# Performance work log

Hardware: AMD Instinct MI355X
Metric: run time of the kernel (lower is better)

The kernel has to match this reference:

```python
import jax, jax.numpy as jnp
import numpy as np

B, L, H = 64, 512, 512          # batch, max_len, hidden_size (code requires H == L)
ITEM = 50001                    # item_num + 1
TEMP = 0.2                      # gumbel-sigmoid temperature
EPS = 1e-20


def setup_inputs() -> dict:
    key = jax.random.key(0)
    ks = jax.random.split(key, 16)
    lin = lambda k: jax.random.normal(k, (L, L), jnp.float32) * (1.0 / np.sqrt(L))
    U = jax.random.uniform(ks[13], (L, H), jnp.float32)
    gumbel = -jnp.log(-jnp.log(U + EPS) + EPS)
    return {
        "positives": jax.random.randint(ks[0], (B, L), 0, ITEM),
        "mask": jax.random.randint(ks[1], (B, L), 0, 2).astype(jnp.int32),
        "item_emb": jax.random.normal(ks[2], (ITEM, H), jnp.float32) * 0.02,
        "pos_emb": jax.random.normal(ks[3], (L, H), jnp.float32) * 0.02,
        "Wz": lin(ks[4]),
        "Wv": lin(ks[5]),
        "Wq": lin(ks[6]),
        "Wk": lin(ks[7]),
        "gamma_q": jax.random.normal(ks[8], (L,), jnp.float32) * 0.02,
        "beta_q": jnp.zeros((L,), jnp.float32),
        "gamma_k": jax.random.normal(ks[9], (L,), jnp.float32) * 0.02,
        "beta_k": jnp.zeros((L,), jnp.float32),
        "sparse_w": jax.random.uniform(ks[10], (L, H), jnp.float32, 0.2, 0.8),
        "gumbel": gumbel,
    }


def reference(positives, mask, item_emb, pos_emb, Wz, Wv, Wq, Wk,
              gamma_q, beta_q, gamma_k, beta_k, sparse_w, gumbel):
    # ---- merge_attn_masks: True = masked ----
    pad = ~(mask.astype(bool))[:, None, :]                 # [B,1,L]
    future = jnp.triu(jnp.ones((L, L), bool), k=1)         # strictly upper
    merged = pad | future[None]                            # [B,L,L]
    attn_mask = (~jnp.eye(L, dtype=bool))[None] & merged   # keep diagonal unmasked

    # ---- embeddings ----
    x = item_emb[positives] + pos_emb[None]                # [B,L,H]

    # ---- GAU-style projections (Linear acts on last dim, y = x @ W^T) ----
    z = jax.nn.silu(x @ Wz.T)                              # [B,L,H]
    v = jax.nn.silu(x @ Wv.T)                              # [B,L,H]
    q = (z @ Wq.T) * gamma_q + beta_q                      # OffsetScale head 0
    k = (z @ Wk.T) * gamma_k + beta_k

    # ---- relu^2 attention with bool mask added then zeroed ----
    m = attn_mask.astype(q.dtype)
    a = jnp.einsum('bld,bmd->blm', q, k) + m               # torch adds bool as 0/1
    a = a * (1.0 - m)                                      # a * ~attn_mask

    # ---- gumbel-sigmoid sparse mask (broadcast [L,L] over batch) ----
    smask = jax.nn.sigmoid((jnp.log(sparse_w / (1.0 - sparse_w)) + gumbel) / TEMP)
    a = smask[None] * a

    a = jnp.square(jax.nn.relu(a)) / (L * H)
    return a @ v                                           # [B,L,H]
```

## Files before the change

### kernel.cpp

```cpp
#include <hip/hip_runtime.h>
#include <hip/hip_fp16.h>
#include <math.h>

typedef _Float16 f16;
typedef unsigned int u32;
typedef _Float16 f16x8 __attribute__((ext_vector_type(8)));
typedef _Float16 f16x4 __attribute__((ext_vector_type(4)));
typedef float    f32x4 __attribute__((ext_vector_type(4)));

constexpr int LEN  = 512;
constexpr int HID  = 512;
constexpr int BATCH = 64;

#define BM 128
#define BN 128
#define BK 64

__device__ __forceinline__ void gload16(const f16* g, f16* l) {
    __builtin_amdgcn_global_load_lds((const __attribute__((address_space(1))) u32*)g,
                                     (__attribute__((address_space(3))) u32*)l,
                                     16, 0, 0);
}

__device__ __forceinline__ float silu_f(float v) {
    return v * __builtin_amdgcn_rcpf(1.f + __expf(-v));
}

#define LDSP 272

__device__ __forceinline__ void stage_pass8(const f16* __restrict__ g, f16* l) {
    const int tid = threadIdx.x;
    const int row = tid >> 2;
    const int sc  = (tid & 3) ^ (row & 3);
    gload16(g + (size_t)row * HID + sc * 8, l + (tid >> 6) * 512);
}

__device__ __forceinline__ void stage_tile8(const f16* __restrict__ A,
                                            const f16* __restrict__ B,
                                            int kt, f16* buf) {
    stage_pass8(A + kt * 32,             buf);
    stage_pass8(A + kt * 32 + 128 * HID, buf + 4096);
    stage_pass8(B + kt * 32,             buf + 8192);
    stage_pass8(B + kt * 32 + 128 * HID, buf + 12288);
}

__device__ __forceinline__ void gemm8_core(const f16* __restrict__ A,
                                           const f16* __restrict__ B,
                                           f16* lds, f32x4 acc[8][4])
{
    const int tid  = threadIdx.x;
    const int lane = tid & 63;
    const int wv   = tid >> 6;
    const int wr   = wv >> 2, wc = wv & 3;
    const int mf   = lane & 15;
    const int slot = ((lane >> 4) ^ (mf & 3)) * 8;
    const int aoff = (wr * 128 + mf) * 32 + slot;
    const int boff = (wc * 64  + mf) * 32 + slot + 8192;

    #pragma unroll
    for (int m = 0; m < 8; ++m)
        #pragma unroll
        for (int n = 0; n < 4; ++n)
            acc[m][n] = (f32x4){0.f, 0.f, 0.f, 0.f};

    stage_tile8(A, B, 0, lds);
    stage_tile8(A, B, 1, lds + 16384);
    asm volatile("s_waitcnt vmcnt(4)" ::: "memory");
    __builtin_amdgcn_s_barrier();

    f16x8 af[4], bf[4];
    #pragma unroll
    for (int kt = 0; kt < 16; ++kt) {
        f16* buf  = lds + (kt % 3) * 16384;
        f16* nbuf = lds + ((kt + 2) % 3) * 16384;
        const bool st = (kt < 14);

        #pragma unroll
        for (int m = 0; m < 4; ++m) af[m] = *(const f16x8*)(buf + aoff + m * 512);
        #pragma unroll
        for (int n = 0; n < 4; ++n) bf[n] = *(const f16x8*)(buf + boff + n * 512);
        if (st) {
            stage_pass8(A + (kt + 2) * 32,             nbuf);
            stage_pass8(A + (kt + 2) * 32 + 128 * HID, nbuf + 4096);
        }
        __builtin_amdgcn_s_barrier();
        asm volatile("s_waitcnt lgkmcnt(0)" ::: "memory");
        __builtin_amdgcn_sched_barrier(0);
        __builtin_amdgcn_s_setprio(1);
        #pragma unroll
        for (int m = 0; m < 4; ++m)
            #pragma unroll
            for (int n = 0; n < 4; ++n)
                acc[m][n] = __builtin_amdgcn_mfma_f32_16x16x32_f16(af[m], bf[n], acc[m][n], 0, 0, 0);
        __builtin_amdgcn_s_setprio(0);
        __builtin_amdgcn_s_barrier();

        #pragma unroll
        for (int m = 0; m < 4; ++m) af[m] = *(const f16x8*)(buf + aoff + (m + 4) * 512);
        if (st) {
            stage_pass8(B + (kt + 2) * 32,             nbuf + 8192);
            stage_pass8(B + (kt + 2) * 32 + 128 * HID, nbuf + 12288);
        }
        __builtin_amdgcn_s_barrier();
        asm volatile("s_waitcnt lgkmcnt(0)" ::: "memory");
        __builtin_amdgcn_sched_barrier(0);
        __builtin_amdgcn_s_setprio(1);
        #pragma unroll
        for (int m = 0; m < 4; ++m)
            #pragma unroll
            for (int n = 0; n < 4; ++n)
                acc[m + 4][n] = __builtin_amdgcn_mfma_f32_16x16x32_f16(af[m], bf[n], acc[m + 4][n], 0, 0, 0);
        __builtin_amdgcn_s_setprio(0);
        if (kt < 14)       asm volatile("s_waitcnt vmcnt(4)" ::: "memory");
        else if (kt == 14) asm volatile("s_waitcnt vmcnt(0)" ::: "memory");
        __builtin_amdgcn_s_barrier();
    }
}

__device__ __forceinline__ void store_tile8(const f16* lds, f16* __restrict__ gout, int ldo) {
    const int tid = threadIdx.x;
    #pragma unroll
    for (int ph = 0; ph < 16; ++ph) {
        const int r = ph * 16 + (tid >> 5);
        const int c = (tid & 31) * 8;
        *(f16x8*)(gout + (size_t)r * ldo + c) = *(const f16x8*)(lds + r * LDSP + c);
    }
}

#define EPI8_IDX() \
    const int lane = threadIdx.x & 63, wv_ = threadIdx.x >> 6;  \
    const int wr = wv_ >> 2, wc = wv_ & 3;                      \
    const int c0 = lane & 15, r0 = (lane >> 4) * 4;

__global__ __launch_bounds__(512, 2) void k_zv8(const f16* __restrict__ x,
                                                const f16* __restrict__ Wzh,
                                                const f16* __restrict__ Wvh,
                                                f16* __restrict__ z,
                                                f16* __restrict__ vt)
{
    __shared__ __align__(16) f16 lds[256 * LDSP];
    const int bid = blockIdx.x;
    const int s  = (bid & 7) + 8 * (bid >> 5);
    const int ci = (bid >> 3) & 3;
    const f16* A; const f16* Bm; f16* gout;
    if (ci < 2) {
        A = x + (size_t)s * 256 * HID;
        Bm = Wzh + (size_t)ci * 256 * HID;
        gout = z + (size_t)s * 256 * HID + ci * 256;
    } else {
        const int ht = ci - 2, b = s >> 1, mt = s & 1;
        A = Wvh + (size_t)ht * 256 * HID;
        Bm = x + ((size_t)b * LEN + mt * 256) * HID;
        gout = vt + (size_t)b * HID * LEN + (size_t)ht * 256 * LEN + mt * 256;
    }
    f32x4 acc[8][4];
    gemm8_core(A, Bm, lds, acc);
    __syncthreads();
    {
        EPI8_IDX();
        #pragma unroll
        for (int m = 0; m < 8; ++m)
            #pragma unroll
            for (int n = 0; n < 4; ++n)
                #pragma unroll
                for (int i = 0; i < 4; ++i) {
                    const int row = wr * 128 + m * 16 + r0 + i;
                    const int col = wc * 64 + n * 16 + c0;
                    lds[row * LDSP + col] = (f16)silu_f(acc[m][n][i]);
                }
    }
    __syncthreads();
    store_tile8(lds, gout, 512);
}

__global__ __launch_bounds__(512, 2) void k_qkp8(const f16* __restrict__ z,
                                                 const f16* __restrict__ Wqh,
                                                 const f16* __restrict__ Wkh,
                                                 const float* __restrict__ gq,
                                                 const float* __restrict__ bq,
                                                 const float* __restrict__ gk,
                                                 const float* __restrict__ bk,
                                                 f16* __restrict__ qh,
                                                 f16* __restrict__ kh)
{
    __shared__ __align__(16) f16 lds[256 * LDSP];
    const int bid = blockIdx.x;
    const int s  = (bid & 7) + 8 * (bid >> 5);
    const int ci = (bid >> 3) & 3;
    const bool isq = ci < 2;
    const int nt = isq ? ci : ci - 2;
    const f16* W = isq ? Wqh : Wkh;
    const float* g  = isq ? gq : gk;
    const float* be = isq ? bq : bk;
    f16* outp = isq ? qh : kh;
    f32x4 acc[8][4];
    gemm8_core(z + (size_t)s * 256 * HID, W + (size_t)nt * 256 * HID, lds, acc);
    __syncthreads();
    {
        EPI8_IDX();
        #pragma unroll
        for (int n = 0; n < 4; ++n) {
            const int col = wc * 64 + n * 16 + c0;
            const int jg = nt * 256 + col;
            const float ga = g[jg], ba = be[jg];
            #pragma unroll
            for (int m = 0; m < 8; ++m)
                #pragma unroll
                for (int i = 0; i < 4; ++i) {
                    const int row = wr * 128 + m * 16 + r0 + i;
                    lds[row * LDSP + col] = (f16)((acc[m][n][i] * ga + ba) * 1024.f);
                }
        }
    }
    __syncthreads();
    store_tile8(lds, outp + (size_t)s * 256 * HID + nt * 256, 512);
}

__device__ __forceinline__ void gemm_core(const f16* __restrict__ A, int lda,
                                          const f16* __restrict__ Bm, int ldb,
                                          int ksteps,
                                          f16* ldsA, f16* ldsB,
                                          f32x4 acc[4][4])
{
    const int tid  = threadIdx.x;
    const int lane = tid & 63;
    const int wv   = tid >> 6;
    const int wr   = wv >> 1, wc = wv & 1;
    const int mf   = lane & 15;
    const int kf   = (lane >> 4) * 8;

    for (int r = 0; r < 4; ++r)
        for (int c = 0; c < 4; ++c)
            acc[r][c] = (f32x4){0.f, 0.f, 0.f, 0.f};

    for (int kt = 0; kt < ksteps; ++kt) {
        const int k0 = kt * BK;
        #pragma unroll
        for (int j = 0; j < 4; ++j) {
            const int cb  = j * 256 + wv * 64;
            const int c   = cb + lane;
            const int row = c >> 3;
            const int col = (c & 7) << 3;
            gload16(A  + (size_t)row * lda + (k0 + col), ldsA + cb * 8);
            gload16(Bm + (size_t)row * ldb + (k0 + col), ldsB + cb * 8);
        }
        __syncthreads();
        #pragma unroll
        for (int kk = 0; kk < BK; kk += 32) {
            f16x8 af[4], bf[4];
            #pragma unroll
            for (int r = 0; r < 4; ++r) {
                af[r] = *(const f16x8*)(ldsA + (wr * 64 + r * 16 + mf) * BK + kk + kf);
                bf[r] = *(const f16x8*)(ldsB + (wc * 64 + r * 16 + mf) * BK + kk + kf);
            }
            #pragma unroll
            for (int r = 0; r < 4; ++r)
                #pragma unroll
                for (int c = 0; c < 4; ++c)
                    acc[r][c] = __builtin_amdgcn_mfma_f32_16x16x32_f16(af[r], bf[c], acc[r][c], 0, 0, 0);
        }
        __syncthreads();
    }
}

#define EPILOGUE_IDX() \
    const int lane = threadIdx.x & 63, wv_ = threadIdx.x >> 6;   \
    const int wr = wv_ >> 1, wc = wv_ & 1;                       \
    const int c0 = lane & 15, r0 = (lane >> 4) * 4;

__device__ __forceinline__ void store_tile_f16(f16* lds, const f16 vals[4][4][4],
                                               f16* __restrict__ gout, int ldo)
{
    const int tid = threadIdx.x;
    EPILOGUE_IDX();
    #pragma unroll
    for (int r = 0; r < 4; ++r)
        #pragma unroll
        for (int c = 0; c < 4; ++c)
            #pragma unroll
            for (int i = 0; i < 4; ++i) {
                const int lr = wr * 64 + r * 16 + r0 + i;
                const int lc = wc * 64 + c * 16 + c0;
                lds[lr * 128 + lc] = vals[r][c][i];
            }
    __syncthreads();
    #pragma unroll
    for (int ph = 0; ph < 8; ++ph) {
        const int row = ph * 16 + (tid >> 4);
        const int col = (tid & 15) * 8;
        *(f16x8*)(gout + (size_t)row * ldo + col) = *(const f16x8*)(lds + row * 128 + col);
    }
}

__constant__ int LT_TAB[10] = {0,1,1,2,2,2,3,3,3,3};
__constant__ int MT_TAB[10] = {0,0,1,0,1,2,0,1,2,3};

__global__ __launch_bounds__(256) void k_qk(const f16* __restrict__ q,
                                            const f16* __restrict__ kmat,
                                            const int* __restrict__ mask,
                                            const float* __restrict__ smask,
                                            f16* __restrict__ p)
{
    const int bid = blockIdx.x;
    const int t = (bid >> 3) % 10;
    const int b = (bid & 7) + 8 * (bid / 80);
    const int lt = LT_TAB[t], mt = MT_TAB[t];
    __shared__ f16 lds[(BM + BN) * BK];
    f32x4 acc[4][4];
    const size_t boff = (size_t)b * LEN * HID;
    gemm_core(q + boff + (size_t)lt * BM * HID, HID,
              kmat + boff + (size_t)mt * BN * HID, HID,
              HID / BK, lds, lds + BM * BK, acc);
    f16 vals[4][4][4];
    {
        EPILOGUE_IDX();
        #pragma unroll
        for (int r = 0; r < 4; ++r)
            #pragma unroll
            for (int c = 0; c < 4; ++c) {
                const int m = mt * BN + wc * 64 + c * 16 + c0;
                const int keepcol = mask[b * LEN + m];
                #pragma unroll
                for (int i = 0; i < 4; ++i) {
                    const int l = lt * BM + wr * 64 + r * 16 + r0 + i;
                    const bool keep = (l == m) || ((m <= l) && (keepcol != 0));
                    float v = keep ? acc[r][c][i] * smask[l * LEN + m] : 0.f;
                    v = fmaxf(v, 0.f);
                    vals[r][c][i] = (f16)(v * v);
                }
            }
    }
    store_tile_f16(lds, vals, p + (size_t)b * LEN * LEN + (size_t)lt * BM * LEN + mt * BN, LEN);
}

__global__ __launch_bounds__(256) void k_pv(const f16* __restrict__ p,
                                            const f16* __restrict__ vt,
                                            float* __restrict__ out)
{
    const int bid = blockIdx.x;
    const int inner = (bid >> 3) & 15;
    const int b = (bid & 7) + 8 * (bid >> 7);
    const int lt = 3 - (inner >> 2), ht = inner & 3;
    __shared__ f16 lds[(BM + BN) * BK];
    f32x4 acc[4][4];
    gemm_core(p + (size_t)b * LEN * LEN + (size_t)lt * BM * LEN, LEN,
              vt + (size_t)b * HID * LEN + (size_t)ht * BN * LEN, LEN,
              (lt + 1) * BM / BK, lds, lds + BM * BK, acc);
    EPILOGUE_IDX();
    const float SCALE = 3.4694469519536142e-18f;
    #pragma unroll
    for (int r = 0; r < 4; ++r)
        #pragma unroll
        for (int c = 0; c < 4; ++c) {
            const int h = ht * BN + wc * 64 + c * 16 + c0;
            #pragma unroll
            for (int i = 0; i < 4; ++i) {
                const int l = lt * BM + wr * 64 + r * 16 + r0 + i;
                out[(size_t)b * LEN * HID + (size_t)l * HID + h] = acc[r][c][i] * SCALE;
            }
        }
}

__global__ __launch_bounds__(256) void k_prep(const int* __restrict__ pos,
                                              const float* __restrict__ item_emb,
                                              const float* __restrict__ pos_emb,
                                              f16* __restrict__ x,
                                              const float* __restrict__ Wz,
                                              const float* __restrict__ Wv,
                                              const float* __restrict__ Wq,
                                              const float* __restrict__ Wk,
                                              f16* __restrict__ Wzh,
                                              f16* __restrict__ Wvh,
                                              f16* __restrict__ Wqh,
                                              f16* __restrict__ Wkh,
                                              const float* __restrict__ sw,
                                              const float* __restrict__ gum,
                                              float* __restrict__ smask)
{
    const int bid = blockIdx.x;
    const int tid = threadIdx.x;
    if (bid < 16384) {
        const int t = bid * 256 + tid;
        const int i = t >> 7;
        const int c = t & 127;
        const int l = i & (LEN - 1);
        const int item = pos[i];
        const float4 a  = ((const float4*)(item_emb + (size_t)item * HID))[c];
        const float4 b4 = ((const float4*)(pos_emb + (size_t)l * HID))[c];
        f16x4 o = { (f16)(a.x + b4.x), (f16)(a.y + b4.y),
                    (f16)(a.z + b4.z), (f16)(a.w + b4.w) };
        *(f16x4*)(x + (size_t)t * 4) = o;
    } else if (bid < 16384 + 1024) {
        const int r = bid - 16384;
        const int w = r >> 8;
        const float* s = (w == 0) ? Wz : (w == 1) ? Wv : (w == 2) ? Wq : Wk;
        f16* d = (w == 0) ? Wzh : (w == 1) ? Wvh : (w == 2) ? Wqh : Wkh;
        const int t = (r & 255) * 256 + tid;
        const float4 v = ((const float4*)s)[t];
        f16x4 o = { (f16)v.x, (f16)v.y, (f16)v.z, (f16)v.w };
        *(f16x4*)(d + (size_t)t * 4) = o;
    } else {
        const int t = (bid - 16384 - 1024) * 256 + tid;
        const float4 w4 = ((const float4*)sw)[t];
        const float4 g4 = ((const float4*)gum)[t];
        float4 o;
        o.x = __builtin_amdgcn_rcpf(1.f + __expf(-(__logf(w4.x / (1.f - w4.x)) + g4.x) * 5.f));
        o.y = __builtin_amdgcn_rcpf(1.f + __expf(-(__logf(w4.y / (1.f - w4.y)) + g4.y) * 5.f));
        o.z = __builtin_amdgcn_rcpf(1.f + __expf(-(__logf(w4.z / (1.f - w4.z)) + g4.z) * 5.f));
        o.w = __builtin_amdgcn_rcpf(1.f + __expf(-(__logf(w4.w / (1.f - w4.w)) + g4.w) * 5.f));
        ((float4*)smask)[t] = o;
    }
}

extern "C" void kernel_launch(void* const* d_in, const int* in_sizes, int n_in,
                              void* d_out, int out_size, void* d_ws, size_t ws_size,
                              hipStream_t stream)
{
    const int*   positives = (const int*)  d_in[0];
    const int*   mask      = (const int*)  d_in[1];
    const float* item_emb  = (const float*)d_in[2];
    const float* pos_emb   = (const float*)d_in[3];
    const float* Wz        = (const float*)d_in[4];
    const float* Wv        = (const float*)d_in[5];
    const float* Wq        = (const float*)d_in[6];
    const float* Wk        = (const float*)d_in[7];
    const float* gamma_q   = (const float*)d_in[8];
    const float* beta_q    = (const float*)d_in[9];
    const float* gamma_k   = (const float*)d_in[10];
    const float* beta_k    = (const float*)d_in[11];
    const float* sparse_w  = (const float*)d_in[12];
    const float* gumbel    = (const float*)d_in[13];
    float* out = (float*)d_out;

    char* ws = (char*)d_ws;
    const size_t BUFB = (size_t)BATCH * LEN * HID * sizeof(f16);
    f16* buf0 = (f16*)ws;
    f16* buf1 = (f16*)(ws + BUFB);
    f16* buf2 = (f16*)(ws + 2 * BUFB);
    f16* Wzh  = (f16*)(ws + 3 * BUFB);
    f16* Wvh  = Wzh + LEN * HID;
    f16* Wqh  = Wvh + LEN * HID;
    f16* Wkh  = Wqh + LEN * HID;
    float* smask = (float*)(Wkh + LEN * HID);
    f16* qh = (f16*)d_out;
    f16* kh = qh + (size_t)BATCH * LEN * HID;

    k_prep<<<16384 + 1024 + 256, 256, 0, stream>>>(
        positives, item_emb, pos_emb, buf0,
        Wz, Wv, Wq, Wk, Wzh, Wvh, Wqh, Wkh,
        sparse_w, gumbel, smask);

    k_zv8<<<512, 512, 0, stream>>>(buf0, Wzh, Wvh, buf1, buf2);

    k_qkp8<<<512, 512, 0, stream>>>(buf1, Wqh, Wkh,
                                    gamma_q, beta_q, gamma_k, beta_k, qh, kh);

    k_qk<<<640, 256, 0, stream>>>(qh, kh, mask, smask, buf0);

    k_pv<<<1024, 256, 0, stream>>>(buf0, buf2, out);
}
```

Before: 354.8 us.

## Deepen projection GEMM pipeline to four stages, change LDS swizzle, split epilogue

The 256x256 projection GEMM core moves from a 3-buffer to a 4-buffer LDS pipeline, prefetching three K-tiles ahead with adjusted vmcnt waits. The XOR swizzle now uses (row>>1)&3, which is meant to reduce LDS bank conflicts on fragment reads. To fit the 128KB staging area, the epilogue is split into two halves that reuse a 128x272 LDS region, with extra barriers between halves. The aim is to hide more global-load latency, at the cost of higher LDS use per block, which may reduce occupancy from two blocks per CU.

New measurement: 355.0 us. No clear change (+0.1%).

```diff
diff --git a/kernel.cpp b/kernel.cpp
--- a/kernel.cpp
+++ b/kernel.cpp
@@ -31,7 +31,7 @@
 __device__ __forceinline__ void stage_pass8(const f16* __restrict__ g, f16* l) {
     const int tid = threadIdx.x;
     const int row = tid >> 2;
-    const int sc  = (tid & 3) ^ (row & 3);
+    const int sc  = (tid & 3) ^ ((row >> 1) & 3);
     gload16(g + (size_t)row * HID + sc * 8, l + (tid >> 6) * 512);
 }
 
@@ -53,7 +53,7 @@
     const int wv   = tid >> 6;
     const int wr   = wv >> 2, wc = wv & 3;
     const int mf   = lane & 15;
-    const int slot = ((lane >> 4) ^ (mf & 3)) * 8;
+    const int slot = ((lane >> 4) ^ ((mf >> 1) & 3)) * 8;
     const int aoff = (wr * 128 + mf) * 32 + slot;
     const int boff = (wc * 64  + mf) * 32 + slot + 8192;
 
@@ -65,23 +65,24 @@
 
     stage_tile8(A, B, 0, lds);
     stage_tile8(A, B, 1, lds + 16384);
-    asm volatile("s_waitcnt vmcnt(4)" ::: "memory");
+    stage_tile8(A, B, 2, lds + 32768);
+    asm volatile("s_waitcnt vmcnt(8)" ::: "memory");
     __builtin_amdgcn_s_barrier();
 
     f16x8 af[4], bf[4];
     #pragma unroll
     for (int kt = 0; kt < 16; ++kt) {
-        f16* buf  = lds + (kt % 3) * 16384;
-        f16* nbuf = lds + ((kt + 2) % 3) * 16384;
-        const bool st = (kt < 14);
+        f16* buf  = lds + (kt & 3) * 16384;
+        f16* nbuf = lds + ((kt + 3) & 3) * 16384;
+        const bool st = (kt < 13);
 
         #pragma unroll
         for (int m = 0; m < 4; ++m) af[m] = *(const f16x8*)(buf + aoff + m * 512);
         #pragma unroll
         for (int n = 0; n < 4; ++n) bf[n] = *(const f16x8*)(buf + boff + n * 512);
         if (st) {
-            stage_pass8(A + (kt + 2) * 32,             nbuf);
-            stage_pass8(A + (kt + 2) * 32 + 128 * HID, nbuf + 4096);
+            stage_pass8(A + (kt + 3) * 32,             nbuf);
+            stage_pass8(A + (kt + 3) * 32 + 128 * HID, nbuf + 4096);
         }
         __builtin_amdgcn_s_barrier();
         asm volatile("s_waitcnt lgkmcnt(0)" ::: "memory");
@@ -98,8 +99,8 @@
         #pragma unroll
         for (int m = 0; m < 4; ++m) af[m] = *(const f16x8*)(buf + aoff + (m + 4) * 512);
         if (st) {
-            stage_pass8(B + (kt + 2) * 32,             nbuf + 8192);
-            stage_pass8(B + (kt + 2) * 32 + 128 * HID, nbuf + 12288);
+            stage_pass8(B + (kt + 3) * 32,             nbuf + 8192);
+            stage_pass8(B + (kt + 3) * 32 + 128 * HID, nbuf + 12288);
         }
         __builtin_amdgcn_s_barrier();
         asm volatile("s_waitcnt lgkmcnt(0)" ::: "memory");
@@ -111,19 +112,10 @@
             for (int n = 0; n < 4; ++n)
                 acc[m + 4][n] = __builtin_amdgcn_mfma_f32_16x16x32_f16(af[m], bf[n], acc[m + 4][n], 0, 0, 0);
         __builtin_amdgcn_s_setprio(0);
-        if (kt < 14)       asm volatile("s_waitcnt vmcnt(4)" ::: "memory");
+        if (kt < 13)       asm volatile("s_waitcnt vmcnt(8)" ::: "memory");
+        else if (kt == 13) asm volatile("s_waitcnt vmcnt(4)" ::: "memory");
         else if (kt == 14) asm volatile("s_waitcnt vmcnt(0)" ::: "memory");
         __builtin_amdgcn_s_barrier();
-    }
-}
-
-__device__ __forceinline__ void store_tile8(const f16* lds, f16* __restrict__ gout, int ldo) {
-    const int tid = threadIdx.x;
-    #pragma unroll
-    for (int ph = 0; ph < 16; ++ph) {
-        const int r = ph * 16 + (tid >> 5);
-        const int c = (tid & 31) * 8;
-        *(f16x8*)(gout + (size_t)r * ldo + c) = *(const f16x8*)(lds + r * LDSP + c);
     }
 }
 
@@ -131,6 +123,17 @@
     const int lane = threadIdx.x & 63, wv_ = threadIdx.x >> 6;  \
     const int wr = wv_ >> 2, wc = wv_ & 3;                      \
     const int c0 = lane & 15, r0 = (lane >> 4) * 4;
+
+__device__ __forceinline__ void store_half8(const f16* lds, f16* __restrict__ gout,
+                                            int ldo, int h) {
+    const int tid = threadIdx.x;
+    #pragma unroll
+    for (int ph = 0; ph < 8; ++ph) {
+        const int r = ph * 16 + (tid >> 5);
+        const int c = (tid & 31) * 8;
+        *(f16x8*)(gout + (size_t)(h * 128 + r) * ldo + c) = *(const f16x8*)(lds + r * LDSP + c);
+    }
+}
 
 __global__ __launch_bounds__(512, 2) void k_zv8(const f16* __restrict__ x,
                                                 const f16* __restrict__ Wzh,
@@ -138,7 +141,7 @@
                                                 f16* __restrict__ z,
                                                 f16* __restrict__ vt)
 {
-    __shared__ __align__(16) f16 lds[256 * LDSP];
+    __shared__ __align__(16) f16 lds[65536];
     const int bid = blockIdx.x;
     const int s  = (bid & 7) + 8 * (bid >> 5);
     const int ci = (bid >> 3) & 3;
@@ -155,22 +158,25 @@
     }
     f32x4 acc[8][4];
     gemm8_core(A, Bm, lds, acc);
-    __syncthreads();
-    {
-        EPI8_IDX();
-        #pragma unroll
-        for (int m = 0; m < 8; ++m)
-            #pragma unroll
-            for (int n = 0; n < 4; ++n)
+    EPI8_IDX();
+    #pragma unroll
+    for (int h = 0; h < 2; ++h) {
+        if (wr == h) {
+            #pragma unroll
+            for (int m = 0; m < 8; ++m)
                 #pragma unroll
-                for (int i = 0; i < 4; ++i) {
-                    const int row = wr * 128 + m * 16 + r0 + i;
-                    const int col = wc * 64 + n * 16 + c0;
-                    lds[row * LDSP + col] = (f16)silu_f(acc[m][n][i]);
-                }
-    }
-    __syncthreads();
-    store_tile8(lds, gout, 512);
+                for (int n = 0; n < 4; ++n)
+                    #pragma unroll
+                    for (int i = 0; i < 4; ++i) {
+                        const int row = m * 16 + r0 + i;
+                        const int col = wc * 64 + n * 16 + c0;
+                        lds[row * LDSP + col] = (f16)silu_f(acc[m][n][i]);
+                    }
+        }
+        __syncthreads();
+        store_half8(lds, gout, 512, h);
+        __syncthreads();
+    }
 }
 
 __global__ __launch_bounds__(512, 2) void k_qkp8(const f16* __restrict__ z,
@@ -183,7 +189,7 @@
                                                  f16* __restrict__ qh,
                                                  f16* __restrict__ kh)
 {
-    __shared__ __align__(16) f16 lds[256 * LDSP];
+    __shared__ __align__(16) f16 lds[65536];
     const int bid = blockIdx.x;
     const int s  = (bid & 7) + 8 * (bid >> 5);
     const int ci = (bid >> 3) & 3;
@@ -195,25 +201,29 @@
     f16* outp = isq ? qh : kh;
     f32x4 acc[8][4];
     gemm8_core(z + (size_t)s * 256 * HID, W + (size_t)nt * 256 * HID, lds, acc);
-    __syncthreads();
-    {
-        EPI8_IDX();
-        #pragma unroll
-        for (int n = 0; n < 4; ++n) {
-            const int col = wc * 64 + n * 16 + c0;
-            const int jg = nt * 256 + col;
-            const float ga = g[jg], ba = be[jg];
-            #pragma unroll
-            for (int m = 0; m < 8; ++m)
+    EPI8_IDX();
+    f16* gbase = outp + (size_t)s * 256 * HID + nt * 256;
+    #pragma unroll
+    for (int h = 0; h < 2; ++h) {
+        if (wr == h) {
+            #pragma unroll
+            for (int n = 0; n < 4; ++n) {
+                const int col = wc * 64 + n * 16 + c0;
+                const int jg = nt * 256 + col;
+                const float ga = g[jg], ba = be[jg];
                 #pragma unroll
-                for (int i = 0; i < 4; ++i) {
-                    const int row = wr * 128 + m * 16 + r0 + i;
-                    lds[row * LDSP + col] = (f16)((acc[m][n][i] * ga + ba) * 1024.f);
-                }
-        }
-    }
-    __syncthreads();
-    store_tile8(lds, outp + (size_t)s * 256 * HID + nt * 256, 512);
+                for (int m = 0; m < 8; ++m)
+                    #pragma unroll
+                    for (int i = 0; i < 4; ++i) {
+                        const int row = m * 16 + r0 + i;
+                        lds[row * LDSP + col] = (f16)((acc[m][n][i] * ga + ba) * 1024.f);
+                    }
+            }
+        }
+        __syncthreads();
+        store_half8(lds, gbase, 512, h);
+        __syncthreads();
+    }
 }
 
 __device__ __forceinline__ void gemm_core(const f16* __restrict__ A, int lda,
```
